# Performance work log

Measured on AMD Instinct MI355X. Metric: run time of the kernel, lower is better.

Reference implementation:

```python
import jax, jax.numpy as jnp
import numpy as np

# Static module config (from Encoder's CropConv layers)
B, CIN, COUT, H, W = 32, 256, 256, 64, 64
K, STRIDE, PAD, DIL = 3, 2, 1, 1
OVERLAP, CENTER = 0, 4


def _build_crop_mask(in_h, out_h, out_w, center_size, overlap):
    """Faithful replica of CropConv's python-loop mask construction,
    including python-slice clamping to L = out_h*out_w."""
    L = out_h * out_w
    crop_start = (in_h - in_h // center_size) // 2 - overlap
    start_idx = in_h * crop_start + crop_start
    crop_size = in_h // center_size + overlap * 2
    not_cropped = crop_start * 2

    def seg_len(a, b):
        # length of python slice [a:b] on an array of length L
        return max(0, min(b, L) - min(a, L))

    segs = []
    for i in range(crop_size):
        if i == 0:
            segs.append(np.ones(seg_len(0, start_idx), bool))
        if i == crop_size - 1:
            segs.append(np.zeros(seg_len(start_idx, start_idx + crop_size), bool))
            segs.append(np.ones(seg_len(start_idx + crop_size, in_h * in_h), bool))
            break
        segs.append(np.zeros(seg_len(start_idx, start_idx + crop_size), bool))
        segs.append(np.ones(seg_len(start_idx + crop_size, start_idx + not_cropped), bool))
        start_idx += in_h
    mask = np.concatenate(segs)
    assert mask.shape[0] == L, (mask.shape[0], L)
    return mask.reshape(out_h, out_w)


def setup_inputs() -> dict:
    key = jax.random.key(0)
    kx, kw = jax.random.split(key)
    x = jax.random.normal(kx, (B, CIN, H, W), dtype=jnp.float32)
    # kaiming_normal(mode='fan_out', nonlinearity='relu'): std = sqrt(2 / (COUT*K*K))
    std = np.sqrt(2.0 / (COUT * K * K)).astype(np.float32)
    weight = jax.random.normal(kw, (COUT, CIN, K, K), dtype=jnp.float32) * std
    return {"x": x, "weight": weight}


def reference(x, weight):
    out_h = (H - K + 2 * PAD) // STRIDE + 1
    out_w = (W - K + 2 * PAD) // STRIDE + 1
    # unfold + matmul == standard convolution; use the efficient fused form
    out = jax.lax.conv_general_dilated(
        x, weight,
        window_strides=(STRIDE, STRIDE),
        padding=[(PAD, PAD), (PAD, PAD)],
        rhs_dilation=(DIL, DIL),
        dimension_numbers=("NCHW", "OIHW", "NCHW"))  # [B, COUT, out_h, out_w]
    mask = jnp.asarray(_build_crop_mask(H, out_h, out_w, CENTER, OVERLAP))
    return jnp.where(mask[None, None, :, :], out, jnp.float32(0.0))
```

## Files before the change

### kernel.cpp

```cpp
#include <hip/hip_runtime.h>


#define B_   32
#define CIN  256
#define COUT 256
#define H_   64
#define W_   64
#define OH   32
#define OW   32

typedef _Float16 f16;
typedef _Float16 half8 __attribute__((ext_vector_type(8)));
typedef float    floatx16 __attribute__((ext_vector_type(16)));

__global__ __launch_bounds__(256) void repack_w_kernel(const float* __restrict__ w,
                                                       f16* __restrict__ rp) {
  int o = blockIdx.x * 256 + threadIdx.x;
  int ci_l = o & 15;
  int tt = o >> 4;
  int co_l = tt & 127; tt >>= 7;
  int khw = tt % 9;    tt /= 9;
  int cc   = tt & 15;  tt >>= 4;
  int co_t = tt;
  int co = co_t * 128 + co_l;
  int ci = cc * 16 + ci_l;
  rp[o] = (f16)w[(co * CIN + ci) * 9 + khw];
}

__global__ __launch_bounds__(256, 2) void conv_mfma_kernel(
    const float* __restrict__ x, const f16* __restrict__ rp,
    float* __restrict__ out) {
  __shared__ f16 ws[9 * 128 * 16];
  __shared__ f16 xs[2 * 9 * 33 * 16];

  const int t    = threadIdx.x;
  const int lane = t & 63;
  const int wave = t >> 6;
  const int wm   = wave >> 1;
  const int wn   = wave & 1;

  const int blk  = blockIdx.x;
  const int b    = blk >> 4;
  const int rem  = blk & 15;
  const int co_t = rem >> 3;
  const int oh0  = (rem & 7) << 2;
  const int ih0  = 2 * oh0 - 1;

  if (t < 144) {
    int r = t >> 4, ci = t & 15;
    xs[((9 + r) * 33 + 0) * 16 + ci] = (f16)0.f;
  }

  floatx16 acc[2][2];
#pragma unroll
  for (int mi = 0; mi < 2; ++mi)
#pragma unroll
    for (int nj = 0; nj < 2; ++nj)
#pragma unroll
      for (int i = 0; i < 16; ++i) acc[mi][nj][i] = 0.f;

  const float* xb  = x + (size_t)b * CIN * H_ * W_;
  const f16*   rpb = rp + (size_t)co_t * (16 * 9 * 128 * 16);

  const int iw = t & 63;
  const int rr = t >> 6;
  const int k0 = (lane >> 5) * 8;
  const int ml = lane & 31;

  for (int cc = 0; cc < 16; ++cc) {
    __syncthreads();
    {
      const half8* src = (const half8*)(rpb + cc * (9 * 128 * 16));
      half8* dst = (half8*)ws;
#pragma unroll
      for (int i = 0; i < 9; ++i) dst[t + i * 256] = src[t + i * 256];
    }
#pragma unroll
    for (int it = 0; it < 3; ++it) {
      int r = rr + it * 4;
      if (r < 9) {
        int ih = ih0 + r;
        const int p   = iw & 1;
        const int idx = (iw + p) >> 1;
#pragma unroll
        for (int g = 0; g < 2; ++g) {
          half8 v;
          if (ih >= 0) {
            const float* xp = xb + ((size_t)(cc * 16 + g * 8) * H_ + ih) * W_ + iw;
#pragma unroll
            for (int c = 0; c < 8; ++c) v[c] = (f16)xp[(size_t)c * H_ * W_];
          } else {
#pragma unroll
            for (int c = 0; c < 8; ++c) v[c] = (f16)0.f;
          }
          *(half8*)&xs[((p * 9 + r) * 33 + idx) * 16 + g * 8] = v;
        }
      }
    }
    __syncthreads();

#pragma unroll
    for (int kh = 0; kh < 3; ++kh) {
#pragma unroll
      for (int kw = 0; kw < 3; ++kw) {
        const int khw = kh * 3 + kw;
        half8 a0 = *(const half8*)&ws[(khw * 128 + wm * 64 + ml) * 16 + k0];
        half8 a1 = *(const half8*)&ws[(khw * 128 + wm * 64 + 32 + ml) * 16 + k0];
        const int p   = (kw & 1) ^ 1;
        const int idx = ml + (kw >> 1);
#pragma unroll
        for (int nj = 0; nj < 2; ++nj) {
          const int r = 2 * (wn * 2 + nj) + kh;
          half8 bf = *(const half8*)&xs[((p * 9 + r) * 33 + idx) * 16 + k0];
          acc[0][nj] = __builtin_amdgcn_mfma_f32_32x32x16_f16(a0, bf, acc[0][nj], 0, 0, 0);
          acc[1][nj] = __builtin_amdgcn_mfma_f32_32x32x16_f16(a1, bf, acc[1][nj], 0, 0, 0);
        }
      }
    }
  }

  const int col = ml;
  const int rowbase = (lane >> 5) * 4;
  float* ob = out + ((size_t)b * COUT + co_t * 128 + wm * 64) * (OH * OW);
#pragma unroll
  for (int mi = 0; mi < 2; ++mi) {
#pragma unroll
    for (int nj = 0; nj < 2; ++nj) {
      const int oh = oh0 + wn * 2 + nj;
#pragma unroll
      for (int r = 0; r < 16; ++r) {
        const int row = mi * 32 + (r & 3) + 8 * (r >> 2) + rowbase;
        ob[(size_t)row * (OH * OW) + oh * OW + col] = acc[mi][nj][r];
      }
    }
  }
}

extern "C" void kernel_launch(void* const* d_in, const int* in_sizes, int n_in,
                              void* d_out, int out_size, void* d_ws, size_t ws_size,
                              hipStream_t stream) {
  const float* x = (const float*)d_in[0];
  const float* w = (const float*)d_in[1];
  float* out = (float*)d_out;
  f16* rp = (f16*)d_ws;

  repack_w_kernel<<<2304, 256, 0, stream>>>(w, rp);
  conv_mfma_kernel<<<512, 256, 0, stream>>>(x, rp, out);
}
```

Baseline: 241.7 us.

## Software-pipeline global loads into registers and double-buffer input tile in LDS

Restructures the channel-chunk loop so the next chunk's input and weight data are loaded from global memory into registers before computing the current chunk. Input tiles are double-buffered in LDS, with the two parity planes offset by a small pad to reduce bank conflicts, and MFMA sections run at raised wave priority. The aim is to hide global load latency behind MFMA work. In exchange it uses many more registers (48 floats plus 9 half8 per thread), which can lower occupancy or cause spills, and it adds an extra barrier per iteration because weights are single-buffered.

New measurement: 221.7 us. 1.09x faster.

```diff
diff --git a/kernel.cpp b/kernel.cpp
--- a/kernel.cpp
+++ b/kernel.cpp
@@ -27,11 +27,15 @@
   rp[o] = (f16)w[(co * CIN + ci) * 9 + khw];
 }
 
+#define XSP   (9 * 33 * 16)
+#define XSP1  (XSP + 8)
+#define XSBUF (XSP1 + XSP)
+
 __global__ __launch_bounds__(256, 2) void conv_mfma_kernel(
     const float* __restrict__ x, const f16* __restrict__ rp,
     float* __restrict__ out) {
   __shared__ f16 ws[9 * 128 * 16];
-  __shared__ f16 xs[2 * 9 * 33 * 16];
+  __shared__ f16 xs[2 * XSBUF];
 
   const int t    = threadIdx.x;
   const int lane = t & 63;
@@ -46,59 +50,82 @@
   const int oh0  = (rem & 7) << 2;
   const int ih0  = 2 * oh0 - 1;
 
-  if (t < 144) {
-    int r = t >> 4, ci = t & 15;
-    xs[((9 + r) * 33 + 0) * 16 + ci] = (f16)0.f;
-  }
-
-  floatx16 acc[2][2];
-#pragma unroll
-  for (int mi = 0; mi < 2; ++mi)
-#pragma unroll
-    for (int nj = 0; nj < 2; ++nj)
-#pragma unroll
-      for (int i = 0; i < 16; ++i) acc[mi][nj][i] = 0.f;
-
   const float* xb  = x + (size_t)b * CIN * H_ * W_;
   const f16*   rpb = rp + (size_t)co_t * (16 * 9 * 128 * 16);
 
-  const int iw = t & 63;
-  const int rr = t >> 6;
-  const int k0 = (lane >> 5) * 8;
-  const int ml = lane & 31;
-
-  for (int cc = 0; cc < 16; ++cc) {
-    __syncthreads();
-    {
-      const half8* src = (const half8*)(rpb + cc * (9 * 128 * 16));
-      half8* dst = (half8*)ws;
-#pragma unroll
-      for (int i = 0; i < 9; ++i) dst[t + i * 256] = src[t + i * 256];
-    }
+  const int iw    = t & 63;
+  const int rr    = t >> 6;
+  const int k0    = (lane >> 5) * 8;
+  const int ml    = lane & 31;
+  const int p_st  = iw & 1;
+  const int idx_st = (iw + p_st) >> 1;
+
+  floatx16 acc[2][2];
+#pragma unroll
+  for (int mi = 0; mi < 2; ++mi)
+#pragma unroll
+    for (int nj = 0; nj < 2; ++nj)
+#pragma unroll
+      for (int i = 0; i < 16; ++i) acc[mi][nj][i] = 0.f;
+
+  float xv[3][2][8];
+  half8 wv[9];
+
+  auto load_x = [&](int cc) {
 #pragma unroll
     for (int it = 0; it < 3; ++it) {
-      int r = rr + it * 4;
+      const int r = rr + it * 4;
       if (r < 9) {
-        int ih = ih0 + r;
-        const int p   = iw & 1;
-        const int idx = (iw + p) >> 1;
+        const int ih = ih0 + r;
+        if (ih >= 0) {
+          const float* xp = xb + (size_t)cc * 16 * (H_ * W_) + (size_t)ih * W_ + iw;
+#pragma unroll
+          for (int g = 0; g < 2; ++g)
+#pragma unroll
+            for (int c = 0; c < 8; ++c)
+              xv[it][g][c] = xp[(size_t)(g * 8 + c) * (H_ * W_)];
+        } else {
+#pragma unroll
+          for (int g = 0; g < 2; ++g)
+#pragma unroll
+            for (int c = 0; c < 8; ++c) xv[it][g][c] = 0.f;
+        }
+      }
+    }
+  };
+
+  auto load_w = [&](int cc) {
+    const half8* src = (const half8*)(rpb + cc * (9 * 128 * 16));
+#pragma unroll
+    for (int i = 0; i < 9; ++i) wv[i] = src[t + i * 256];
+  };
+
+  auto write_x = [&](int nxt) {
+    f16* xd = &xs[nxt * XSBUF + (p_st ? XSP1 : 0)];
+#pragma unroll
+    for (int it = 0; it < 3; ++it) {
+      const int r = rr + it * 4;
+      if (r < 9) {
 #pragma unroll
         for (int g = 0; g < 2; ++g) {
           half8 v;
-          if (ih >= 0) {
-            const float* xp = xb + ((size_t)(cc * 16 + g * 8) * H_ + ih) * W_ + iw;
-#pragma unroll
-            for (int c = 0; c < 8; ++c) v[c] = (f16)xp[(size_t)c * H_ * W_];
-          } else {
-#pragma unroll
-            for (int c = 0; c < 8; ++c) v[c] = (f16)0.f;
-          }
-          *(half8*)&xs[((p * 9 + r) * 33 + idx) * 16 + g * 8] = v;
+#pragma unroll
+          for (int c = 0; c < 8; ++c) v[c] = (f16)xv[it][g][c];
+          *(half8*)&xd[(r * 33 + idx_st) * 16 + g * 8] = v;
         }
       }
     }
-    __syncthreads();
-
+  };
+
+  auto write_w = [&]() {
+    half8* dst = (half8*)ws;
+#pragma unroll
+    for (int i = 0; i < 9; ++i) dst[t + i * 256] = wv[i];
+  };
+
+  auto compute = [&](int cur) {
+    const f16* xc = &xs[cur * XSBUF];
+    __builtin_amdgcn_s_setprio(1);
 #pragma unroll
     for (int kh = 0; kh < 3; ++kh) {
 #pragma unroll
@@ -106,18 +133,47 @@
         const int khw = kh * 3 + kw;
         half8 a0 = *(const half8*)&ws[(khw * 128 + wm * 64 + ml) * 16 + k0];
         half8 a1 = *(const half8*)&ws[(khw * 128 + wm * 64 + 32 + ml) * 16 + k0];
-        const int p   = (kw & 1) ^ 1;
+        const int pp  = (kw & 1) ^ 1;
         const int idx = ml + (kw >> 1);
+        const f16* xpl = xc + (pp ? XSP1 : 0);
 #pragma unroll
         for (int nj = 0; nj < 2; ++nj) {
           const int r = 2 * (wn * 2 + nj) + kh;
-          half8 bf = *(const half8*)&xs[((p * 9 + r) * 33 + idx) * 16 + k0];
+          half8 bf = *(const half8*)&xpl[(r * 33 + idx) * 16 + k0];
           acc[0][nj] = __builtin_amdgcn_mfma_f32_32x32x16_f16(a0, bf, acc[0][nj], 0, 0, 0);
           acc[1][nj] = __builtin_amdgcn_mfma_f32_32x32x16_f16(a1, bf, acc[1][nj], 0, 0, 0);
         }
       }
     }
+    __builtin_amdgcn_s_setprio(0);
+  };
+
+  if (t < 144) {
+    const int r = t >> 4, ci = t & 15;
+    xs[0 * XSBUF + XSP1 + (r * 33) * 16 + ci] = (f16)0.f;
+    xs[1 * XSBUF + XSP1 + (r * 33) * 16 + ci] = (f16)0.f;
   }
+
+  load_x(0);
+  load_w(0);
+  write_x(0);
+  write_w();
+  __syncthreads();
+
+  int cur = 0;
+#pragma unroll 1
+  for (int cc = 0; cc < 15; ++cc) {
+    load_x(cc + 1);
+    load_w(cc + 1);
+    __builtin_amdgcn_sched_barrier(0);
+    compute(cur);
+    write_x(cur ^ 1);
+    __syncthreads();
+    write_w();
+    __syncthreads();
+    cur ^= 1;
+  }
+  compute(cur);
 
   const int col = ml;
   const int rowbase = (lane >> 5) * 4;
```
